# Kernel optimization log

Measured on AMD Instinct MI355X. Metric: run time of the kernel, lower is better.

The kernel has to match this reference:

```python
import jax, jax.numpy as jnp
import numpy as np

# Lorenz parameters (fixed in LorenzSDE.__init__)
SIGMA = 10.0
RHO = 28.0
BETA = 8.0 / 3.0
NOISE = 2.0      # σ diffusion scale (diffusion = σ * I_3, additive)
T = 0.05
DT = 0.01
N_STEPS = 5      # T / DT, ConstantStepSize (no stepsize_controller passed)
BATCH = 4194304


def _drift(y):
    # y: [..., 3] Lorenz vector field
    x_, y_, z_ = y[..., 0], y[..., 1], y[..., 2]
    return jnp.stack(
        [SIGMA * (y_ - x_), x_ * (RHO - z_) - y_, x_ * y_ - BETA * z_], axis=-1
    )


def setup_inputs() -> dict:
    key = jax.random.key(0)
    k1, k2, k3 = jax.random.split(key, 3)
    x = jax.random.normal(k1, (BATCH, 3), dtype=jnp.float32)
    # standard normals; scaled inside reference to Brownian increment / Levy area
    dW = jax.random.normal(k2, (BATCH, N_STEPS, 3), dtype=jnp.float32)
    dH = jax.random.normal(k3, (BATCH, N_STEPS, 3), dtype=jnp.float32)
    return {"x": x, "dW": dW, "dH": dH}


def reference(x, dW, dH):
    # ShARK (Shifted Additive-noise Runge-Kutta), strong order 1.5 for additive
    # noise, two drift evaluations per step (diffrax.ShARK with constant steps):
    #   z1 = y + g*H
    #   z2 = y + (5/6)*h*f(z1) + g*((5/6)*W + H)
    #   y1 = y + h*(0.4*f(z1) + 0.6*f(z2)) + g*W
    # where W ~ N(0, h I), H (space-time Levy area) ~ N(0, h/12 I), g = NOISE*I.
    dt = jnp.float32(DT)
    gW = jnp.moveaxis(dW, 1, 0) * (NOISE * jnp.sqrt(dt))          # [n, B, 3]
    gH = jnp.moveaxis(dH, 1, 0) * (NOISE * jnp.sqrt(dt / 12.0))   # [n, B, 3]

    def step(y, wh):
        w, h = wh
        z1 = y + h
        f1 = _drift(z1)
        z2 = y + (5.0 / 6.0) * dt * f1 + (5.0 / 6.0) * w + h
        f2 = _drift(z2)
        y1 = y + dt * (0.4 * f1 + 0.6 * f2) + w
        return y1, None

    yT, _ = jax.lax.scan(step, x, (gW, gH))
    return yT  # [B, 3] final state (sol.ys saves t1 only)
```

## Files before the change

### kernel.cpp

```cpp
#include <hip/hip_runtime.h>
#include <stdint.h>


#define NSTEPS 5
#define BLOCK 256
#define WPB 4
#define TILE 64

__device__ __forceinline__ void gll16(const float4* g, float* l) {
    __builtin_amdgcn_global_load_lds(
        (const __attribute__((address_space(1))) void*)g,
        (__attribute__((address_space(3))) void*)l,
        16, 0, 0);
}

__global__ __launch_bounds__(BLOCK) void lorenz_shark(
    const float* __restrict__ x,
    const float* __restrict__ dW,
    const float* __restrict__ dH,
    float* __restrict__ out)
{
    __shared__ float s_w[WPB][TILE * 15];
    __shared__ float s_h[WPB][TILE * 15];
    __shared__ float s_x[WPB][TILE * 3];

    const int lane = threadIdx.x & 63;
    const int wv   = threadIdx.x >> 6;
    const long long ptBase = ((long long)blockIdx.x * WPB + wv) * TILE;

    const float4* gw = (const float4*)(dW + ptBase * 15);
    const float4* gh = (const float4*)(dH + ptBase * 15);
    const float4* gx = (const float4*)(x  + ptBase * 3);

#pragma unroll
    for (int k = 0; k < 3; ++k) {
        gll16(gw + lane + k * 64, &s_w[wv][k * 256]);
        gll16(gh + lane + k * 64, &s_h[wv][k * 256]);
    }
    if (lane < 48) {
        gll16(gw + lane + 192, &s_w[wv][768]);
        gll16(gh + lane + 192, &s_h[wv][768]);
        gll16(gx + lane,       &s_x[wv][0]);
    }
    asm volatile("s_waitcnt vmcnt(0)" ::: "memory");
    __builtin_amdgcn_sched_barrier(0);
    __builtin_amdgcn_wave_barrier();

    float a = s_x[wv][3 * lane + 0];
    float b = s_x[wv][3 * lane + 1];
    float c = s_x[wv][3 * lane + 2];

    const float cW    = 0.2f;
    const float cH    = 0.05773502691896258f;
    const float dt    = 0.01f;
    const float c56   = 5.0f / 6.0f;
    const float c56dt = c56 * dt;
    const float SIGMA = 10.0f;
    const float RHO   = 28.0f;
    const float BETA  = 8.0f / 3.0f;

#pragma unroll
    for (int n = 0; n < NSTEPS; ++n) {
        const int w0 = 15 * lane + 3 * n;
        const float wa = s_w[wv][w0 + 0] * cW;
        const float wb = s_w[wv][w0 + 1] * cW;
        const float wc = s_w[wv][w0 + 2] * cW;
        const float ha = s_h[wv][w0 + 0] * cH;
        const float hb = s_h[wv][w0 + 1] * cH;
        const float hc = s_h[wv][w0 + 2] * cH;

        const float z1a = a + ha, z1b = b + hb, z1c = c + hc;
        const float f1a = SIGMA * (z1b - z1a);
        const float f1b = z1a * (RHO - z1c) - z1b;
        const float f1c = z1a * z1b - BETA * z1c;

        const float z2a = a + c56dt * f1a + c56 * wa + ha;
        const float z2b = b + c56dt * f1b + c56 * wb + hb;
        const float z2c = c + c56dt * f1c + c56 * wc + hc;
        const float f2a = SIGMA * (z2b - z2a);
        const float f2b = z2a * (RHO - z2c) - z2b;
        const float f2c = z2a * z2b - BETA * z2c;

        a = a + dt * (0.4f * f1a + 0.6f * f2a) + wa;
        b = b + dt * (0.4f * f1b + 0.6f * f2b) + wb;
        c = c + dt * (0.4f * f1c + 0.6f * f2c) + wc;
    }

    s_x[wv][3 * lane + 0] = a;
    s_x[wv][3 * lane + 1] = b;
    s_x[wv][3 * lane + 2] = c;
    __builtin_amdgcn_wave_barrier();

    float4* lx = (float4*)s_x[wv];
    float4* go = (float4*)(out + ptBase * 3);
    if (lane < 48) go[lane] = lx[lane];
}

extern "C" void kernel_launch(void* const* d_in, const int* in_sizes, int n_in,
                              void* d_out, int out_size, void* d_ws, size_t ws_size,
                              hipStream_t stream) {
    const float* x  = (const float*)d_in[0];
    const float* dW = (const float*)d_in[1];
    const float* dH = (const float*)d_in[2];
    float* out = (float*)d_out;

    const int batch   = in_sizes[0] / 3;
    const int nblocks = batch / (WPB * TILE);

    hipLaunchKernelGGL(lorenz_shark, dim3(nblocks), dim3(BLOCK), 0, stream,
                       x, dW, dH, out);
}
```

Baseline: 520.3 us.

## Use persistent grid with double-buffered LDS prefetch of next tile

The kernel moves from one tile per wave with a one-shot launch to a fixed grid of 512 blocks. Each wave loops over strided tiles and stages the next tile's dW/dH/x into a second LDS buffer with global_load_lds while it integrates the current one. The goal is to overlap memory fetch with compute and cut block launch and tail overhead in this bandwidth-heavy kernel. The cost is double the LDS per block, which limits how many blocks fit on a CU. It also depends on a hand-set vmcnt(9) wait count being correct.

```diff
diff --git a/kernel.cpp b/kernel.cpp
--- a/kernel.cpp
+++ b/kernel.cpp
@@ -6,6 +6,7 @@
 #define BLOCK 256
 #define WPB 4
 #define TILE 64
+#define GRID 512
 
 __device__ __forceinline__ void gll16(const float4* g, float* l) {
     __builtin_amdgcn_global_load_lds(
@@ -18,37 +19,40 @@
     const float* __restrict__ x,
     const float* __restrict__ dW,
     const float* __restrict__ dH,
-    float* __restrict__ out)
+    float* __restrict__ out,
+    int batch)
 {
-    __shared__ float s_w[WPB][TILE * 15];
-    __shared__ float s_h[WPB][TILE * 15];
-    __shared__ float s_x[WPB][TILE * 3];
+    __shared__ float s_w[2][WPB][TILE * 15];
+    __shared__ float s_h[2][WPB][TILE * 15];
+    __shared__ float s_x[2][WPB][TILE * 3];
 
-    const int lane = threadIdx.x & 63;
-    const int wv   = threadIdx.x >> 6;
-    const long long ptBase = ((long long)blockIdx.x * WPB + wv) * TILE;
+    const int lane   = threadIdx.x & 63;
+    const int wv     = threadIdx.x >> 6;
+    const int waveId = blockIdx.x * WPB + wv;
+    const int nWaves = GRID * WPB;
+    const int nTiles = batch / TILE;
+    const int NTbase = nTiles / nWaves;
+    const int rem    = nTiles - NTbase * nWaves;
+    const int NT     = NTbase + (waveId < rem ? 1 : 0);
 
-    const float4* gw = (const float4*)(dW + ptBase * 15);
-    const float4* gh = (const float4*)(dH + ptBase * 15);
-    const float4* gx = (const float4*)(x  + ptBase * 3);
-
+    auto stage = [&](int buf, long long tile) {
+        const float4* gw = (const float4*)(dW + tile * (TILE * 15));
+        const float4* gh = (const float4*)(dH + tile * (TILE * 15));
+        const float4* gx = (const float4*)(x  + tile * (TILE * 3));
+        float* lw = s_w[buf][wv];
+        float* lh = s_h[buf][wv];
+        float* lx = s_x[buf][wv];
 #pragma unroll
-    for (int k = 0; k < 3; ++k) {
-        gll16(gw + lane + k * 64, &s_w[wv][k * 256]);
-        gll16(gh + lane + k * 64, &s_h[wv][k * 256]);
-    }
-    if (lane < 48) {
-        gll16(gw + lane + 192, &s_w[wv][768]);
-        gll16(gh + lane + 192, &s_h[wv][768]);
-        gll16(gx + lane,       &s_x[wv][0]);
-    }
-    asm volatile("s_waitcnt vmcnt(0)" ::: "memory");
-    __builtin_amdgcn_sched_barrier(0);
-    __builtin_amdgcn_wave_barrier();
-
-    float a = s_x[wv][3 * lane + 0];
-    float b = s_x[wv][3 * lane + 1];
-    float c = s_x[wv][3 * lane + 2];
+        for (int k = 0; k < 3; ++k) {
+            gll16(gw + lane + k * 64, lw + k * 256);
+            gll16(gh + lane + k * 64, lh + k * 256);
+        }
+        if (lane < 48) {
+            gll16(gw + lane + 192, lw + 768);
+            gll16(gh + lane + 192, lh + 768);
+            gll16(gx + lane,       lx);
+        }
+    };
 
     const float cW    = 0.2f;
     const float cH    = 0.05773502691896258f;
@@ -59,41 +63,64 @@
     const float RHO   = 28.0f;
     const float BETA  = 8.0f / 3.0f;
 
+    if (NT <= 0) return;
+    stage(0, (long long)waveId);
+
+    for (int t = 0; t < NT; ++t) {
+        if (t + 1 < NT) {
+            stage((t + 1) & 1, (long long)waveId + (long long)(t + 1) * nWaves);
+            asm volatile("s_waitcnt vmcnt(9)" ::: "memory");
+        } else {
+            asm volatile("s_waitcnt vmcnt(0)" ::: "memory");
+        }
+        __builtin_amdgcn_sched_barrier(0);
+
+        const int buf = t & 1;
+        const float* sw = s_w[buf][wv];
+        const float* sh = s_h[buf][wv];
+        float*       sx = s_x[buf][wv];
+
+        float a = sx[3 * lane + 0];
+        float b = sx[3 * lane + 1];
+        float c = sx[3 * lane + 2];
+
 #pragma unroll
-    for (int n = 0; n < NSTEPS; ++n) {
-        const int w0 = 15 * lane + 3 * n;
-        const float wa = s_w[wv][w0 + 0] * cW;
-        const float wb = s_w[wv][w0 + 1] * cW;
-        const float wc = s_w[wv][w0 + 2] * cW;
-        const float ha = s_h[wv][w0 + 0] * cH;
-        const float hb = s_h[wv][w0 + 1] * cH;
-        const float hc = s_h[wv][w0 + 2] * cH;
+        for (int n = 0; n < NSTEPS; ++n) {
+            const int w0 = 15 * lane + 3 * n;
+            const float wa = sw[w0 + 0] * cW;
+            const float wb = sw[w0 + 1] * cW;
+            const float wc = sw[w0 + 2] * cW;
+            const float ha = sh[w0 + 0] * cH;
+            const float hb = sh[w0 + 1] * cH;
+            const float hc = sh[w0 + 2] * cH;
 
-        const float z1a = a + ha, z1b = b + hb, z1c = c + hc;
-        const float f1a = SIGMA * (z1b - z1a);
-        const float f1b = z1a * (RHO - z1c) - z1b;
-        const float f1c = z1a * z1b - BETA * z1c;
+            const float z1a = a + ha, z1b = b + hb, z1c = c + hc;
+            const float f1a = SIGMA * (z1b - z1a);
+            const float f1b = z1a * (RHO - z1c) - z1b;
+            const float f1c = z1a * z1b - BETA * z1c;
 
-        const float z2a = a + c56dt * f1a + c56 * wa + ha;
-        const float z2b = b + c56dt * f1b + c56 * wb + hb;
-        const float z2c = c + c56dt * f1c + c56 * wc + hc;
-        const float f2a = SIGMA * (z2b - z2a);
-        const float f2b = z2a * (RHO - z2c) - z2b;
-        const float f2c = z2a * z2b - BETA * z2c;
+            const float z2a = a + c56dt * f1a + c56 * wa + ha;
+            const float z2b = b + c56dt * f1b + c56 * wb + hb;
+            const float z2c = c + c56dt * f1c + c56 * wc + hc;
+            const float f2a = SIGMA * (z2b - z2a);
+            const float f2b = z2a * (RHO - z2c) - z2b;
+            const float f2c = z2a * z2b - BETA * z2c;
 
-        a = a + dt * (0.4f * f1a + 0.6f * f2a) + wa;
-        b = b + dt * (0.4f * f1b + 0.6f * f2b) + wb;
-        c = c + dt * (0.4f * f1c + 0.6f * f2c) + wc;
+            a = a + dt * (0.4f * f1a + 0.6f * f2a) + wa;
+            b = b + dt * (0.4f * f1b + 0.6f * f2b) + wb;
+            c = c + dt * (0.4f * f1c + 0.6f * f2c) + wc;
+        }
+
+        sx[3 * lane + 0] = a;
+        sx[3 * lane + 1] = b;
+        sx[3 * lane + 2] = c;
+        __builtin_amdgcn_wave_barrier();
+
+        const long long tile = (long long)waveId + (long long)t * nWaves;
+        float4* go = (float4*)(out + tile * (TILE * 3));
+        const float4* lx4 = (const float4*)sx;
+        if (lane < 48) go[lane] = lx4[lane];
     }
-
-    s_x[wv][3 * lane + 0] = a;
-    s_x[wv][3 * lane + 1] = b;
-    s_x[wv][3 * lane + 2] = c;
-    __builtin_amdgcn_wave_barrier();
-
-    float4* lx = (float4*)s_x[wv];
-    float4* go = (float4*)(out + ptBase * 3);
-    if (lane < 48) go[lane] = lx[lane];
 }
 
 extern "C" void kernel_launch(void* const* d_in, const int* in_sizes, int n_in,
@@ -104,9 +131,8 @@
     const float* dH = (const float*)d_in[2];
     float* out = (float*)d_out;
 
-    const int batch   = in_sizes[0] / 3;
-    const int nblocks = batch / (WPB * TILE);
+    const int batch = in_sizes[0] / 3;
 
-    hipLaunchKernelGGL(lorenz_shark, dim3(nblocks), dim3(BLOCK), 0, stream,
-                       x, dW, dH, out);
+    hipLaunchKernelGGL(lorenz_shark, dim3(GRID), dim3(BLOCK), 0, stream,
+                       x, dW, dH, out, batch);
 }
```

Result: no change. 524.0 us (+0.7%).
